# Kernel optimization log

Measured on AMD Instinct MI355X. Metric: run time of the kernel, lower is better.

Reference implementation:

```python
import jax, jax.numpy as jnp
import numpy as np

HIDDEN = 2048
HEADS = 16
HEAD_DIM = HIDDEN // HEADS

def setup_inputs() -> dict:
    key = jax.random.key(0)
    ks = jax.random.split(key, 9)
    B, S = 1, 4096
    scale = 1.0 / np.sqrt(HIDDEN)
    x = jax.random.normal(ks[0], (B, S, HIDDEN), dtype=jnp.float32)
    Wq = jax.random.normal(ks[1], (HIDDEN, HIDDEN), dtype=jnp.float32) * scale
    Wk = jax.random.normal(ks[2], (HIDDEN, HIDDEN), dtype=jnp.float32) * scale
    Wv = jax.random.normal(ks[3], (HIDDEN, HIDDEN), dtype=jnp.float32) * scale
    Wo = jax.random.normal(ks[4], (HIDDEN, HIDDEN), dtype=jnp.float32) * scale
    bq = jax.random.normal(ks[5], (HIDDEN,), dtype=jnp.float32) * 0.01
    bk = jax.random.normal(ks[6], (HIDDEN,), dtype=jnp.float32) * 0.01
    bv = jax.random.normal(ks[7], (HIDDEN,), dtype=jnp.float32) * 0.01
    bo = jax.random.normal(ks[8], (HIDDEN,), dtype=jnp.float32) * 0.01
    return {"x": x, "Wq": Wq, "bq": bq, "Wk": Wk, "bk": bk, "Wv": Wv, "bv": bv, "Wo": Wo, "bo": bo}

def reference(x, Wq, bq, Wk, bk, Wv, bv, Wo, bo):
    B, S, D = x.shape
    H, Hd = HEADS, HEAD_DIM
    # projections (nn.Linear: x @ W^T + b)
    Q = (x @ Wq.T + bq).reshape(B, S, H, Hd).transpose(0, 2, 1, 3)  # [B,H,S,Hd]
    K = (x @ Wk.T + bk).reshape(B, S, H, Hd).transpose(0, 2, 1, 3)
    V = (x @ Wv.T + bv).reshape(B, S, H, Hd).transpose(0, 2, 1, 3)
    scores = jnp.einsum('bhqd,bhkd->bhqk', Q, K) / jnp.sqrt(jnp.float32(Hd))
    attn = jax.nn.softmax(scores, axis=-1)
    out = jnp.einsum('bhqk,bhkd->bhqd', attn, V)  # [B,H,S,Hd]
    out = out.transpose(0, 2, 1, 3).reshape(B, S, D)
    return out @ Wo.T + bo
```

## Files before the change

kernel.cpp:

```cpp
#include <hip/hip_runtime.h>

#define S_LEN  4096
#define DMODEL 2048
#define NHEADS 16
#define HDIM   128

typedef __bf16 bf16x8 __attribute__((ext_vector_type(8)));
typedef __bf16 bf16x2 __attribute__((ext_vector_type(2)));
typedef float  f32x4  __attribute__((ext_vector_type(4)));
typedef float  f32x16 __attribute__((ext_vector_type(16)));

__device__ __forceinline__ unsigned short f2b(float f) {
    unsigned int u = __float_as_uint(f);
    unsigned int r = (u + 0x7fffu + ((u >> 16) & 1u)) >> 16;
    return (unsigned short)r;
}

__device__ __forceinline__ unsigned int pkbf16(float a, float b) {
#if __has_builtin(__builtin_amdgcn_cvt_pk_bf16_f32)
    bf16x2 t = __builtin_amdgcn_cvt_pk_bf16_f32(a, b);
    return *(unsigned int*)&t;
#else
    return (unsigned int)f2b(a) | ((unsigned int)f2b(b) << 16);
#endif
}

__device__ __forceinline__ f32x4 mfma16(bf16x8 a, bf16x8 b, f32x4 c) {
    return __builtin_amdgcn_mfma_f32_16x16x32_bf16(a, b, c, 0, 0, 0);
}

__device__ __forceinline__ f32x16 mfma32(bf16x8 a, bf16x8 b, f32x16 c) {
    return __builtin_amdgcn_mfma_f32_32x32x16_bf16(a, b, c, 0, 0, 0);
}

__device__ __forceinline__ void ldg2lds16(const void* g, void* l) {
    __builtin_amdgcn_global_load_lds(
        (__attribute__((address_space(1))) void*)(void*)g,
        (__attribute__((address_space(3))) void*)l, 16, 0, 0);
}

__global__ __launch_bounds__(256) void cvt_all(
    const float* __restrict__ x,
    const float* __restrict__ w0, const float* __restrict__ w1,
    const float* __restrict__ w2, const float* __restrict__ w3,
    unsigned short* __restrict__ dst)
{
    int i = blockIdx.x * 256 + threadIdx.x;
    const float* src; int off;
    if (i < (1 << 21)) { src = x; off = i; }
    else {
        int j = i - (1 << 21);
        int sel = j >> 20; off = j & ((1 << 20) - 1);
        src = (sel == 0) ? w0 : (sel == 1) ? w1 : (sel == 2) ? w2 : w3;
    }
    float4 v = ((const float4*)src)[off];
    uint2 h;
    h.x = pkbf16(v.x, v.y); h.y = pkbf16(v.z, v.w);
    ((uint2*)dst)[i] = h;
}

__global__ __launch_bounds__(256, 2) void gemm_qkv(
    const unsigned short* __restrict__ xb,
    const unsigned short* __restrict__ Wqb, const float* __restrict__ bq,
    const unsigned short* __restrict__ Wkb, const float* __restrict__ bk,
    const unsigned short* __restrict__ Wvb, const float* __restrict__ bv,
    unsigned short* __restrict__ Qb, unsigned short* __restrict__ Kb,
    unsigned short* __restrict__ Vb)
{
    const int id  = blockIdx.x + 16 * (blockIdx.y + 32 * blockIdx.z);
    const int swz = (id & 7) * 192 + (id >> 3);
    const int n0 = (swz & 15) * 128;
    const int m0 = ((swz >> 4) & 31) * 128;
    const int z  = swz >> 9;

    const unsigned short* B = (z == 0) ? Wqb : (z == 1) ? Wkb : Wvb;
    const float* bias        = (z == 0) ? bq  : (z == 1) ? bk  : bv;
    unsigned short* C        = (z == 0) ? Qb  : (z == 1) ? Kb  : Vb;
    const float oscale = (z == 0) ? 0.12751743f : 1.0f;

    __shared__ alignas(16) unsigned short As[128 * 32];
    __shared__ alignas(16) unsigned short Bs[128 * 32];

    const int tid = threadIdx.x;
    const int w = tid >> 6, lane = tid & 63, lo = lane & 15, qd = lane >> 4;
    const int wm = (w >> 1) * 64, wn = (w & 1) * 64;
    const int rsel = lane >> 2, csel = (lane & 3) * 8;

    f32x4 acc[4][4] = {};

    for (int k0 = 0; k0 < DMODEL; k0 += 32) {
#pragma unroll
        for (int i = 0; i < 2; i++) {
            int c = w * 2 + i;
            ldg2lds16(&xb[(size_t)(m0 + c * 16 + rsel) * DMODEL + k0 + csel],
                      &As[c * 512]);
            ldg2lds16(&B [(size_t)(n0 + c * 16 + rsel) * DMODEL + k0 + csel],
                      &Bs[c * 512]);
        }
        __syncthreads();

        bf16x8 af[4], bfr[4];
#pragma unroll
        for (int i = 0; i < 4; i++)
            af[i] = *(const bf16x8*)&As[(wm + i * 16 + lo) * 32 + qd * 8];
#pragma unroll
        for (int j = 0; j < 4; j++)
            bfr[j] = *(const bf16x8*)&Bs[(wn + j * 16 + lo) * 32 + qd * 8];
#pragma unroll
        for (int i = 0; i < 4; i++)
#pragma unroll
            for (int j = 0; j < 4; j++)
                acc[i][j] = mfma16(af[i], bfr[j], acc[i][j]);
        __syncthreads();
    }

#pragma unroll
    for (int j = 0; j < 4; j++) {
        int n = n0 + wn + j * 16 + lo;
        float bv_ = bias[n];
#pragma unroll
        for (int i = 0; i < 4; i++) {
#pragma unroll
            for (int r = 0; r < 4; r++) {
                int m = m0 + wm + i * 16 + qd * 4 + r;
                C[(size_t)m * DMODEL + n] = f2b((acc[i][j][r] + bv_) * oscale);
            }
        }
    }
}

__global__ __launch_bounds__(256, 2) void gemm_out(
    const unsigned short* __restrict__ Aatt, const unsigned short* __restrict__ Wob,
    const float* __restrict__ bo, float* __restrict__ out)
{
    const int id  = blockIdx.x + 16 * blockIdx.y;
    const int swz = (id & 7) * 64 + (id >> 3);
    const int n0 = (swz & 15) * 128;
    const int m0 = (swz >> 4) * 128;

    __shared__ alignas(16) unsigned short As[128 * 32];
    __shared__ alignas(16) unsigned short Bs[128 * 32];

    const int tid = threadIdx.x;
    const int w = tid >> 6, lane = tid & 63, lo = lane & 15, qd = lane >> 4;
    const int wm = (w >> 1) * 64, wn = (w & 1) * 64;
    const int rsel = lane >> 2, csel = (lane & 3) * 8;

    f32x4 acc[4][4] = {};

    for (int k0 = 0; k0 < DMODEL; k0 += 32) {
#pragma unroll
        for (int i = 0; i < 2; i++) {
            int c = w * 2 + i;
            ldg2lds16(&Aatt[(size_t)(m0 + c * 16 + rsel) * DMODEL + k0 + csel],
                      &As[c * 512]);
            ldg2lds16(&Wob [(size_t)(n0 + c * 16 + rsel) * DMODEL + k0 + csel],
                      &Bs[c * 512]);
        }
        __syncthreads();

        bf16x8 af[4], bfr[4];
#pragma unroll
        for (int i = 0; i < 4; i++)
            af[i] = *(const bf16x8*)&As[(wm + i * 16 + lo) * 32 + qd * 8];
#pragma unroll
        for (int j = 0; j < 4; j++)
            bfr[j] = *(const bf16x8*)&Bs[(wn + j * 16 + lo) * 32 + qd * 8];
#pragma unroll
        for (int i = 0; i < 4; i++)
#pragma unroll
            for (int j = 0; j < 4; j++)
                acc[i][j] = mfma16(af[i], bfr[j], acc[i][j]);
        __syncthreads();
    }

#pragma unroll
    for (int j = 0; j < 4; j++) {
        int n = n0 + wn + j * 16 + lo;
        float bv_ = bo[n];
#pragma unroll
        for (int i = 0; i < 4; i++) {
#pragma unroll
            for (int r = 0; r < 4; r++) {
                int m = m0 + wm + i * 16 + qd * 4 + r;
                out[(size_t)m * DMODEL + n] = acc[i][j][r] + bv_;
            }
        }
    }
}

__global__ __launch_bounds__(256) void transpose_v(
    const unsigned short* __restrict__ Vb, unsigned short* __restrict__ Vt)
{
    __shared__ unsigned short tile[64 * 67];
    const int s0 = blockIdx.x * 64;
    const int d0 = blockIdx.y * 64;
    const int tid = threadIdx.x;
#pragma unroll
    for (int i = 0; i < 2; i++) {
        int chunk = tid + i * 256;
        int r = chunk >> 3, c8 = (chunk & 7) * 8;
        uint4 v = *(const uint4*)&Vb[(size_t)(s0 + r) * DMODEL + d0 + c8];
        const unsigned short* p = (const unsigned short*)&v;
#pragma unroll
        for (int j = 0; j < 8; j++) tile[r * 67 + c8 + j] = p[j];
    }
    __syncthreads();
#pragma unroll
    for (int i = 0; i < 2; i++) {
        int chunk = tid + i * 256;
        int r = chunk >> 3, c8 = (chunk & 7) * 8;
        unsigned short tmp[8];
#pragma unroll
        for (int j = 0; j < 8; j++) tmp[j] = tile[(c8 + j) * 67 + r];
        *(uint4*)&Vt[(size_t)(d0 + r) * S_LEN + s0 + c8] = *(uint4*)tmp;
    }
}

__global__ __launch_bounds__(256, 2) void attn_kernel(
    const unsigned short* __restrict__ Qb, const unsigned short* __restrict__ Kb,
    const unsigned short* __restrict__ Vt, unsigned short* __restrict__ Ob)
{
    const int id = blockIdx.x;
    const int xcd = id & 7, slot = id >> 3;
    const int h  = (xcd << 1) | (slot >> 6);
    const int q0 = (slot & 63) * 64;

    __shared__ alignas(16) unsigned char smem[65536];
    unsigned short* Ks0  = (unsigned short*)smem;
    unsigned short* Ks1  = (unsigned short*)(smem + 16384);
    unsigned short* Vts0 = (unsigned short*)(smem + 32768);
    unsigned short* Vts1 = (unsigned short*)(smem + 49152);
    float* Of = (float*)smem;
    float* Lf = (float*)(smem + 32768);

    const int tid = threadIdx.x;
    const int w = tid >> 6, lane = tid & 63;
    const int qw = w >> 1, kw = w & 1;
    const int l31 = lane & 31, hi = lane >> 5;
    const int sw7 = l31 & 7;

    bf16x8 qf[8];
    {
        const unsigned short* qrow =
            &Qb[(size_t)(q0 + qw * 32 + l31) * DMODEL + h * HDIM];
#pragma unroll
        for (int sl = 0; sl < 8; sl++)
            qf[sl] = *(const bf16x8*)&qrow[sl * 16 + hi * 8];
    }

    f32x16 o_acc[4] = {};
    float l_run = 0.f;

    const int krow = kw * 32 + l31;

#define STAGE_K(dst_, key0_)                                                  \
    {                                                                         \
        _Pragma("unroll")                                                     \
        for (int i = 0; i < 4; i++) {                                         \
            int r = w * 16 + i * 4 + (lane >> 4);                             \
            int c = (lane & 15) ^ (r & 7);                                    \
            ldg2lds16(&Kb[(size_t)((key0_) + r) * DMODEL + h * HDIM + c * 8], \
                      &(dst_)[(w * 16 + i * 4) * 128]);                       \
        }                                                                     \
    }
#define STAGE_V(dst_, key0_)                                                  \
    {                                                                         \
        _Pragma("unroll")                                                     \
        for (int i = 0; i < 4; i++) {                                         \
            int r = w * 32 + i * 8 + (lane >> 3);                             \
            int c = (lane & 7) ^ (r & 7);                                     \
            ldg2lds16(&Vt[(size_t)(h * HDIM + r) * S_LEN + (key0_) + c * 8],  \
                      &(dst_)[(w * 32 + i * 8) * 64]);                        \
        }                                                                     \
    }

#define QKT(KsC, SOUT)                                                        \
    {                                                                         \
        f32x16 sa_ = {}, sb_ = {};                                            \
        _Pragma("unroll")                                                     \
        for (int sl = 0; sl < 8; sl += 2) {                                   \
            bf16x8 kfa = *(const bf16x8*)                                     \
                &(KsC)[krow * 128 + (((2 * sl + hi) ^ sw7) * 8)];             \
            bf16x8 kfb = *(const bf16x8*)                                     \
                &(KsC)[krow * 128 + (((2 * (sl + 1) + hi) ^ sw7) * 8)];       \
            sa_ = mfma32(kfa, qf[sl], sa_);                                   \
            sb_ = mfma32(kfb, qf[sl + 1], sb_);                               \
        }                                                                     \
        SOUT = sa_ + sb_;                                                     \
    }

#define SMPV(SIN, VtsP)                                                       \
    {                                                                         \
        bf16x8 pa0, pa1;                                                      \
        float ls = 0.f;                                                       \
        _Pragma("unroll")                                                     \
        for (int k2 = 0; k2 < 2; k2++) {                                      \
            float e0 = __builtin_amdgcn_exp2f(SIN[8 * k2 + 0]);               \
            float e1 = __builtin_amdgcn_exp2f(SIN[8 * k2 + 1]);               \
            float e2 = __builtin_amdgcn_exp2f(SIN[8 * k2 + 2]);               \
            float e3 = __builtin_amdgcn_exp2f(SIN[8 * k2 + 3]);               \
            float e4 = __builtin_amdgcn_exp2f(SIN[8 * k2 + 4]);               \
            float e5 = __builtin_amdgcn_exp2f(SIN[8 * k2 + 5]);               \
            float e6 = __builtin_amdgcn_exp2f(SIN[8 * k2 + 6]);               \
            float e7 = __builtin_amdgcn_exp2f(SIN[8 * k2 + 7]);               \
            ls += ((e0 + e1) + (e2 + e3)) + ((e4 + e5) + (e6 + e7));          \
            unsigned int c0 = pkbf16(e0, e1);                                 \
            unsigned int c1 = pkbf16(e2, e3);                                 \
            unsigned int c2 = pkbf16(e4, e5);                                 \
            unsigned int c3 = pkbf16(e6, e7);                                 \
            asm("v_permlane32_swap_b32 %0, %1" : "+v"(c0), "+v"(c2));         \
            asm("v_permlane32_swap_b32 %0, %1" : "+v"(c1), "+v"(c3));         \
            uint4 u; u.x = c0; u.y = c1; u.z = c2; u.w = c3;                  \
            if (k2 == 0) pa0 = *(bf16x8*)&u; else pa1 = *(bf16x8*)&u;         \
        }                                                                     \
        l_run += ls;                                                          \
        _Pragma("unroll")                                                     \
        for (int k2 = 0; k2 < 2; k2++) {                                      \
            const int gch = 4 * kw + 2 * k2 + hi;                             \
            bf16x8 pf = (k2 == 0) ? pa0 : pa1;                                \
            _Pragma("unroll")                                                 \
            for (int dt = 0; dt < 4; dt++) {                                  \
                bf16x8 vf = *(const bf16x8*)                                  \
                    &(VtsP)[(dt * 32 + l31) * 64 + ((gch ^ sw7) * 8)];        \
                o_acc[dt] = mfma32(pf, vf, o_acc[dt]);                        \
            }                                                                 \
        }                                                                     \
    }

#define ATTN_STEP(t_, KC, KN, VC, VP, SIN, SOUT)                              \
    {                                                                         \
        if ((t_) + 1 < S_LEN / 64) STAGE_K(KN, ((t_) + 1) * 64);              \
        STAGE_V(VC, (t_) * 64);                                               \
        __builtin_amdgcn_s_setprio(1);                                        \
        QKT(KC, SOUT);                                                        \
        SMPV(SIN, VP);                                                        \
        __builtin_amdgcn_s_setprio(0);                                        \
        __syncthreads();                                                      \
    }

    f32x16 sP, sQ;

    STAGE_K(Ks0, 0);
    __syncthreads();
    STAGE_K(Ks1, 64);
    STAGE_V(Vts0, 0);
    QKT(Ks0, sP);
    __syncthreads();

    for (int t = 1; t < S_LEN / 64 - 1; t += 2) {
        ATTN_STEP(t,     Ks1, Ks0, Vts1, Vts0, sP, sQ);
        ATTN_STEP(t + 1, Ks0, Ks1, Vts0, Vts1, sQ, sP);
    }
    ATTN_STEP(S_LEN / 64 - 1, Ks1, Ks0, Vts1, Vts0, sP, sQ);

    SMPV(sQ, Vts1);

#undef ATTN_STEP
#undef SMPV
#undef QKT
#undef STAGE_K
#undef STAGE_V

    float l = l_run + __shfl_xor(l_run, 32);

    if (kw == 1) {
#pragma unroll
        for (int dt = 0; dt < 4; dt++)
#pragma unroll
            for (int r = 0; r < 16; r++) {
                int row = (r & 3) + 8 * (r >> 2) + 4 * hi;
                Of[(qw * 32 + row) * 128 + dt * 32 + l31] = o_acc[dt][r];
            }
    }
    if (hi == 0) Lf[(qw * 2 + kw) * 32 + l31] = l;
    __syncthreads();

    if (kw == 0) {
        float linv[16];
#pragma unroll
        for (int r = 0; r < 16; r++) {
            int row = (r & 3) + 8 * (r >> 2) + 4 * hi;
            linv[r] = 1.0f / (Lf[(qw * 2 + 0) * 32 + row] +
                              Lf[(qw * 2 + 1) * 32 + row]);
        }
#pragma unroll
        for (int dt = 0; dt < 4; dt++)
#pragma unroll
            for (int r = 0; r < 16; r++) {
                int row = (r & 3) + 8 * (r >> 2) + 4 * hi;
                float v = o_acc[dt][r] + Of[(qw * 32 + row) * 128 + dt * 32 + l31];
                Ob[(size_t)(q0 + qw * 32 + row) * DMODEL + h * HDIM + dt * 32 + l31]
                    = f2b(v * linv[r]);
            }
    }
}

extern "C" void kernel_launch(void* const* d_in, const int* in_sizes, int n_in,
                              void* d_out, int out_size, void* d_ws, size_t ws_size,
                              hipStream_t stream)
{
    const float* x  = (const float*)d_in[0];
    const float* Wq = (const float*)d_in[1];
    const float* bq = (const float*)d_in[2];
    const float* Wk = (const float*)d_in[3];
    const float* bk = (const float*)d_in[4];
    const float* Wv = (const float*)d_in[5];
    const float* bv = (const float*)d_in[6];
    const float* Wo = (const float*)d_in[7];
    const float* bo = (const float*)d_in[8];
    float* out = (float*)d_out;

    const size_t N = (size_t)S_LEN * DMODEL;
    const size_t W = (size_t)DMODEL * DMODEL;
    unsigned short* Qb  = (unsigned short*)d_ws;
    unsigned short* Kb  = Qb + N;
    unsigned short* Vb  = Kb + N;
    unsigned short* xbv = Vb + N;
    unsigned short* Wqb = xbv + N;
    unsigned short* Wkb = Wqb + W;
    unsigned short* Wvb = Wkb + W;
    unsigned short* Wob = Wvb + W;
    unsigned short* Vt  = xbv;
    unsigned short* Ob  = Vb;

    cvt_all<<<24576, 256, 0, stream>>>(x, Wq, Wk, Wv, Wo, xbv);

    gemm_qkv<<<dim3(DMODEL / 128, S_LEN / 128, 3), 256, 0, stream>>>(
        xbv, Wqb, bq, Wkb, bk, Wvb, bv, Qb, Kb, Vb);

    transpose_v<<<dim3(S_LEN / 64, DMODEL / 64), 256, 0, stream>>>(Vb, Vt);

    attn_kernel<<<1024, 256, 0, stream>>>(Qb, Kb, Vt, Ob);

    gemm_out<<<dim3(DMODEL / 128, S_LEN / 128), 256, 0, stream>>>(Ob, Wob, bo, out);
}
```

Baseline: 483.8 us.

## Fuse V transpose into QKV GEMM epilogue and compute row sums via MFMA

The QKV GEMM now writes V directly in transposed layout (d-major, sequence-contiguous), so the separate transpose_v kernel and its extra read/write pass over V are removed. Workspace aliasing changes so that Ob reuses the x buffer. Separately, the attention kernel no longer sums exp values in scalar VALU code; it accumulates row sums by multiplying the P fragments with a ones vector on the matrix cores. This moves VALU work onto the MFMA pipe at the cost of two extra MFMAs per step and an extra accumulator register block. The transposed V stores are 8-byte strided writes, which may coalesce less well than the old epilogue.

```diff
diff --git a/kernel.cpp b/kernel.cpp
--- a/kernel.cpp
+++ b/kernel.cpp
@@ -65,7 +65,7 @@
     const unsigned short* __restrict__ Wkb, const float* __restrict__ bk,
     const unsigned short* __restrict__ Wvb, const float* __restrict__ bv,
     unsigned short* __restrict__ Qb, unsigned short* __restrict__ Kb,
-    unsigned short* __restrict__ Vb)
+    unsigned short* __restrict__ Vt)
 {
     const int id  = blockIdx.x + 16 * (blockIdx.y + 32 * blockIdx.z);
     const int swz = (id & 7) * 192 + (id >> 3);
@@ -75,7 +75,6 @@
 
     const unsigned short* B = (z == 0) ? Wqb : (z == 1) ? Wkb : Wvb;
     const float* bias        = (z == 0) ? bq  : (z == 1) ? bk  : bv;
-    unsigned short* C        = (z == 0) ? Qb  : (z == 1) ? Kb  : Vb;
     const float oscale = (z == 0) ? 0.12751743f : 1.0f;
 
     __shared__ alignas(16) unsigned short As[128 * 32];
@@ -114,16 +113,34 @@
         __syncthreads();
     }
 
-#pragma unroll
-    for (int j = 0; j < 4; j++) {
-        int n = n0 + wn + j * 16 + lo;
-        float bv_ = bias[n];
-#pragma unroll
-        for (int i = 0; i < 4; i++) {
-#pragma unroll
-            for (int r = 0; r < 4; r++) {
-                int m = m0 + wm + i * 16 + qd * 4 + r;
-                C[(size_t)m * DMODEL + n] = f2b((acc[i][j][r] + bv_) * oscale);
+    if (z == 2) {
+#pragma unroll
+        for (int j = 0; j < 4; j++) {
+            int n = n0 + wn + j * 16 + lo;
+            float bv_ = bias[n];
+#pragma unroll
+            for (int i = 0; i < 4; i++) {
+                int ms = m0 + wm + i * 16 + qd * 4;
+                unsigned short tmp[4];
+#pragma unroll
+                for (int r = 0; r < 4; r++)
+                    tmp[r] = f2b(acc[i][j][r] + bv_);
+                *(uint2*)&Vt[(size_t)n * S_LEN + ms] = *(uint2*)tmp;
+            }
+        }
+    } else {
+        unsigned short* C = (z == 0) ? Qb : Kb;
+#pragma unroll
+        for (int j = 0; j < 4; j++) {
+            int n = n0 + wn + j * 16 + lo;
+            float bv_ = bias[n];
+#pragma unroll
+            for (int i = 0; i < 4; i++) {
+#pragma unroll
+                for (int r = 0; r < 4; r++) {
+                    int m = m0 + wm + i * 16 + qd * 4 + r;
+                    C[(size_t)m * DMODEL + n] = f2b((acc[i][j][r] + bv_) * oscale);
+                }
             }
         }
     }
@@ -189,34 +206,6 @@
     }
 }
 
-__global__ __launch_bounds__(256) void transpose_v(
-    const unsigned short* __restrict__ Vb, unsigned short* __restrict__ Vt)
-{
-    __shared__ unsigned short tile[64 * 67];
-    const int s0 = blockIdx.x * 64;
-    const int d0 = blockIdx.y * 64;
-    const int tid = threadIdx.x;
-#pragma unroll
-    for (int i = 0; i < 2; i++) {
-        int chunk = tid + i * 256;
-        int r = chunk >> 3, c8 = (chunk & 7) * 8;
-        uint4 v = *(const uint4*)&Vb[(size_t)(s0 + r) * DMODEL + d0 + c8];
-        const unsigned short* p = (const unsigned short*)&v;
-#pragma unroll
-        for (int j = 0; j < 8; j++) tile[r * 67 + c8 + j] = p[j];
-    }
-    __syncthreads();
-#pragma unroll
-    for (int i = 0; i < 2; i++) {
-        int chunk = tid + i * 256;
-        int r = chunk >> 3, c8 = (chunk & 7) * 8;
-        unsigned short tmp[8];
-#pragma unroll
-        for (int j = 0; j < 8; j++) tmp[j] = tile[(c8 + j) * 67 + r];
-        *(uint4*)&Vt[(size_t)(d0 + r) * S_LEN + s0 + c8] = *(uint4*)tmp;
-    }
-}
-
 __global__ __launch_bounds__(256, 2) void attn_kernel(
     const unsigned short* __restrict__ Qb, const unsigned short* __restrict__ Kb,
     const unsigned short* __restrict__ Vt, unsigned short* __restrict__ Ob)
@@ -249,8 +238,12 @@
             qf[sl] = *(const bf16x8*)&qrow[sl * 16 + hi * 8];
     }
 
+    bf16x8 onesb;
+#pragma unroll
+    for (int i = 0; i < 8; i++) onesb[i] = (__bf16)1.0f;
+
     f32x16 o_acc[4] = {};
-    float l_run = 0.f;
+    f32x16 o_l = {};
 
     const int krow = kw * 32 + l31;
 
@@ -293,7 +286,6 @@
 #define SMPV(SIN, VtsP)                                                       \
     {                                                                         \
         bf16x8 pa0, pa1;                                                      \
-        float ls = 0.f;                                                       \
         _Pragma("unroll")                                                     \
         for (int k2 = 0; k2 < 2; k2++) {                                      \
             float e0 = __builtin_amdgcn_exp2f(SIN[8 * k2 + 0]);               \
@@ -304,7 +296,6 @@
             float e5 = __builtin_amdgcn_exp2f(SIN[8 * k2 + 5]);               \
             float e6 = __builtin_amdgcn_exp2f(SIN[8 * k2 + 6]);               \
             float e7 = __builtin_amdgcn_exp2f(SIN[8 * k2 + 7]);               \
-            ls += ((e0 + e1) + (e2 + e3)) + ((e4 + e5) + (e6 + e7));          \
             unsigned int c0 = pkbf16(e0, e1);                                 \
             unsigned int c1 = pkbf16(e2, e3);                                 \
             unsigned int c2 = pkbf16(e4, e5);                                 \
@@ -314,7 +305,8 @@
             uint4 u; u.x = c0; u.y = c1; u.z = c2; u.w = c3;                  \
             if (k2 == 0) pa0 = *(bf16x8*)&u; else pa1 = *(bf16x8*)&u;         \
         }                                                                     \
-        l_run += ls;                                                          \
+        o_l = mfma32(pa0, onesb, o_l);                                        \
+        o_l = mfma32(pa1, onesb, o_l);                                        \
         _Pragma("unroll")                                                     \
         for (int k2 = 0; k2 < 2; k2++) {                                      \
             const int gch = 4 * kw + 2 * k2 + hi;                             \
@@ -362,8 +354,6 @@
 #undef STAGE_K
 #undef STAGE_V
 
-    float l = l_run + __shfl_xor(l_run, 32);
-
     if (kw == 1) {
 #pragma unroll
         for (int dt = 0; dt < 4; dt++)
@@ -373,7 +363,13 @@
                 Of[(qw * 32 + row) * 128 + dt * 32 + l31] = o_acc[dt][r];
             }
     }
-    if (hi == 0) Lf[(qw * 2 + kw) * 32 + l31] = l;
+    if (l31 == 0) {
+#pragma unroll
+        for (int r = 0; r < 16; r++) {
+            int row = (r & 3) + 8 * (r >> 2) + 4 * hi;
+            Lf[(qw * 2 + kw) * 32 + row] = o_l[r];
+        }
+    }
     __syncthreads();
 
     if (kw == 0) {
@@ -415,21 +411,18 @@
     const size_t W = (size_t)DMODEL * DMODEL;
     unsigned short* Qb  = (unsigned short*)d_ws;
     unsigned short* Kb  = Qb + N;
-    unsigned short* Vb  = Kb + N;
-    unsigned short* xbv = Vb + N;
+    unsigned short* Vt  = Kb + N;
+    unsigned short* xbv = Vt + N;
     unsigned short* Wqb = xbv + N;
     unsigned short* Wkb = Wqb + W;
     unsigned short* Wvb = Wkb + W;
     unsigned short* Wob = Wvb + W;
-    unsigned short* Vt  = xbv;
-    unsigned short* Ob  = Vb;
+    unsigned short* Ob  = xbv;
 
     cvt_all<<<24576, 256, 0, stream>>>(x, Wq, Wk, Wv, Wo, xbv);
 
     gemm_qkv<<<dim3(DMODEL / 128, S_LEN / 128, 3), 256, 0, stream>>>(
-        xbv, Wqb, bq, Wkb, bk, Wvb, bv, Qb, Kb, Vb);
-
-    transpose_v<<<dim3(S_LEN / 64, DMODEL / 64), 256, 0, stream>>>(Vb, Vt);
+        xbv, Wqb, bq, Wkb, bk, Wvb, bv, Qb, Kb, Vt);
 
     attn_kernel<<<1024, 256, 0, stream>>>(Qb, Kb, Vt, Ob);
 
```

After: 504.3 us. 1.04x slower.
